# Optimization experiments

Hardware: AMD Instinct MI355X
Metric: run time of the kernel (lower is better)

Reference implementation:

```python
import jax, jax.numpy as jnp
import numpy as np


def setup_inputs() -> dict:
    key = jax.random.key(0)
    k0, k1, k2 = jax.random.split(key, 3)
    B, N, C = 2, 2048, 1024
    x = jax.random.normal(k0, (B, N, C), jnp.float32)
    W_qkv = jax.random.normal(k1, (3 * C, C), jnp.float32) * 0.02
    b_qkv = jnp.zeros((3 * C,), jnp.float32)
    W_out = jax.random.normal(k2, (C, C), jnp.float32) * 0.02
    b_out = jnp.zeros((C,), jnp.float32)
    return {"x": x, "W_qkv": W_qkv, "b_qkv": b_qkv, "W_out": W_out, "b_out": b_out, "n_heads": 16}


def reference(x, W_qkv, b_qkv, W_out, b_out, n_heads):
    B, N, C = x.shape
    dk = C // n_heads
    scale = 1.0 / np.sqrt(dk)
    # qkv projection -> (3, B, H, N, dk)
    qkv = (x @ W_qkv.T + b_qkv).reshape(B, N, 3, n_heads, dk).transpose(2, 0, 3, 1, 4)
    q, k, v = qkv[0], qkv[1], qkv[2]
    attn_all = jnp.einsum('bhqd,bhkd->bhqk', q, k) * scale  # (B,H,N,N)
    # sparsity measure per query row: max - mean
    M = jnp.max(attn_all, axis=-1) - jnp.mean(attn_all, axis=-1)  # (B,H,N)
    n_top = max(1, min(int(N * 0.25), N - 1))
    _, top_idx = jax.lax.top_k(M, n_top)  # (B,H,n_top)
    # keep[b,h,q] = True iff query row q is among top rows (vectorized scatter,
    # replaces the original per-(b,h) python loop)
    b_idx = jnp.arange(B)[:, None, None]
    h_idx = jnp.arange(n_heads)[None, :, None]
    keep = jnp.zeros((B, n_heads, N), bool).at[b_idx, h_idx, top_idx].set(True)
    # non-top query rows are fully masked to -1e9 (as in masked_fill)
    attn = jnp.where(keep[..., None], attn_all, jnp.float32(-1e9))
    attn = jax.nn.softmax(attn, axis=-1)
    # dropout is identity in eval mode
    out = jnp.einsum('bhqk,bhkd->bhqd', attn, v)
    out = out.transpose(0, 2, 1, 3).reshape(B, N, C)
    return out @ W_out.T + b_out
```

## Files before the change

kernel.cpp:

```cpp
#include <hip/hip_runtime.h>
#include <math.h>

typedef unsigned short u16;
typedef __attribute__((ext_vector_type(8))) short short8v;
typedef __attribute__((ext_vector_type(4))) float f32x4;

constexpr int B  = 2;
constexpr int N  = 2048;
constexpr int C  = 1024;
constexpr int H  = 16;
constexpr int DK = 64;
constexpr int NTOP = 512;
constexpr float SCALE = 0.125f;
constexpr int   BAND_CAP = 1024;
constexpr float BAND_EPS = 2e-3f;
constexpr int   CSEG = 16;

__device__ __forceinline__ void gload16(const u16* g, u16* l) {
    __builtin_amdgcn_global_load_lds(
        (const __attribute__((address_space(1))) unsigned int*)g,
        (__attribute__((address_space(3))) unsigned int*)l,
        16, 0, 0);
}

__device__ __forceinline__ u16 bf16_rne(float x) {
    unsigned u = __float_as_uint(x);
    unsigned r = u + 0x7fffu + ((u >> 16) & 1u);
    return (u16)(r >> 16);
}

__global__ __launch_bounds__(256) void convert_hilo(
    const float* __restrict__ src, u16* __restrict__ hi, u16* __restrict__ lo, int n)
{
    int i = (blockIdx.x * 256 + threadIdx.x) * 4;
    if (i >= n) return;
    float4 v = *(const float4*)&src[i];
    u16 h0 = bf16_rne(v.x), h1 = bf16_rne(v.y), h2 = bf16_rne(v.z), h3 = bf16_rne(v.w);
    float f0 = __uint_as_float((unsigned)h0 << 16);
    float f1 = __uint_as_float((unsigned)h1 << 16);
    float f2 = __uint_as_float((unsigned)h2 << 16);
    float f3 = __uint_as_float((unsigned)h3 << 16);
    *(ushort4*)&hi[i] = make_ushort4(h0, h1, h2, h3);
    *(ushort4*)&lo[i] = make_ushort4(bf16_rne(v.x - f0), bf16_rne(v.y - f1),
                                     bf16_rne(v.z - f2), bf16_rne(v.w - f3));
}

__global__ __launch_bounds__(256) void convert_hilo2(
    const float* __restrict__ a, const float* __restrict__ b,
    u16* __restrict__ ah, u16* __restrict__ al,
    u16* __restrict__ bh_, u16* __restrict__ bl_, int n)
{
    const float* src = blockIdx.y ? b : a;
    u16* hi = blockIdx.y ? bh_ : ah;
    u16* lo = blockIdx.y ? bl_ : al;
    int i = (blockIdx.x * 256 + threadIdx.x) * 4;
    if (i >= n) return;
    float4 v = *(const float4*)&src[i];
    u16 h0 = bf16_rne(v.x), h1 = bf16_rne(v.y), h2 = bf16_rne(v.z), h3 = bf16_rne(v.w);
    float f0 = __uint_as_float((unsigned)h0 << 16);
    float f1 = __uint_as_float((unsigned)h1 << 16);
    float f2 = __uint_as_float((unsigned)h2 << 16);
    float f3 = __uint_as_float((unsigned)h3 << 16);
    *(ushort4*)&hi[i] = make_ushort4(h0, h1, h2, h3);
    *(ushort4*)&lo[i] = make_ushort4(bf16_rne(v.x - f0), bf16_rne(v.y - f1),
                                     bf16_rne(v.z - f2), bf16_rne(v.w - f3));
}

__global__ __launch_bounds__(256) void convert_hilo_T(
    const float* __restrict__ v, u16* __restrict__ th, u16* __restrict__ tl)
{
    constexpr int LS = 68;
    __shared__ u16 Sh[64 * LS], Sl[64 * LS];
    const int bh = blockIdx.y;
    const int kt = blockIdx.x * 64;
    const int tid = threadIdx.x;
    #pragma unroll
    for (int p = 0; p < 4; ++p) {
        int idx = tid * 4 + p * 1024;
        int key = idx >> 6, d = idx & 63;
        float4 x4 = *(const float4*)&v[((size_t)bh * N + kt + key) * DK + d];
        float xs[4] = {x4.x, x4.y, x4.z, x4.w};
        ushort4 hh, ll;
        u16* hp = (u16*)&hh; u16* lp = (u16*)&ll;
        #pragma unroll
        for (int j = 0; j < 4; ++j) {
            u16 h = bf16_rne(xs[j]);
            hp[j] = h;
            lp[j] = bf16_rne(xs[j] - __uint_as_float((unsigned)h << 16));
        }
        *(ushort4*)&Sh[key * LS + d] = hh;
        *(ushort4*)&Sl[key * LS + d] = ll;
    }
    __syncthreads();
    const int d = tid >> 2, seg = tid & 3;
    u16 bufh[16], bufl[16];
    #pragma unroll
    for (int i = 0; i < 16; ++i) {
        bufh[i] = Sh[(seg * 16 + i) * LS + d];
        bufl[i] = Sl[(seg * 16 + i) * LS + d];
    }
    size_t oa = ((size_t)bh * DK + d) * N + kt + seg * 16;
    *(uint4*)&th[oa] = ((uint4*)bufh)[0];
    *(uint4*)&th[oa + 8] = ((uint4*)bufh)[1];
    *(uint4*)&tl[oa] = ((uint4*)bufl)[0];
    *(uint4*)&tl[oa + 8] = ((uint4*)bufl)[1];
}

template <int MODE>
__global__ __launch_bounds__(256) void gemm_mfma(
    const u16* __restrict__ Ahi, const u16* __restrict__ Alo,
    const u16* __restrict__ Bhi, const u16* __restrict__ Blo,
    const float* __restrict__ bias, float* __restrict__ out,
    float* __restrict__ qb, float* __restrict__ kb, float* __restrict__ vb,
    int K)
{
    __shared__ __align__(16) u16 Ah[128 * 32], Al[128 * 32];
    __shared__ __align__(16) u16 Bh[128 * 32], Bl[128 * 32];

    const int tid = threadIdx.x;
    const int m0 = blockIdx.y * 128;
    const int n0 = blockIdx.x * 128;
    const int lane = tid & 63;
    const int wave = tid >> 6;
    const int wr = wave >> 1, wc = wave & 1;
    const int fr = lane & 15, sl = lane >> 4;

    const u16* gsrc = (wave == 0) ? Ahi + (size_t)m0 * K
                    : (wave == 1) ? Alo + (size_t)m0 * K
                    : (wave == 2) ? Bhi + (size_t)n0 * K
                                  : Blo + (size_t)n0 * K;
    u16* lbase = (wave == 0) ? Ah : (wave == 1) ? Al : (wave == 2) ? Bh : Bl;

    f32x4 acc[4][4] = {};

    for (int k0 = 0; k0 < K; k0 += 32) {
        __syncthreads();
        #pragma unroll
        for (int i = 0; i < 8; ++i) {
            int c = i * 64 + lane;
            int row = c >> 2, sp = c & 3;
            int gs = sp ^ ((row >> 1) & 3);
            gload16(gsrc + (size_t)row * K + k0 + gs * 8, lbase + i * 512);
        }
        __syncthreads();

        short8v afh[4], afl[4], bfh[4], bfl[4];
        #pragma unroll
        for (int m = 0; m < 4; ++m) {
            int row = wr * 64 + m * 16 + fr;
            int off = row * 32 + ((sl ^ ((row >> 1) & 3)) * 8);
            afh[m] = *(const short8v*)&Ah[off];
            afl[m] = *(const short8v*)&Al[off];
        }
        #pragma unroll
        for (int n = 0; n < 4; ++n) {
            int row = wc * 64 + n * 16 + fr;
            int off = row * 32 + ((sl ^ ((row >> 1) & 3)) * 8);
            bfh[n] = *(const short8v*)&Bh[off];
            bfl[n] = *(const short8v*)&Bl[off];
        }
        #pragma unroll
        for (int m = 0; m < 4; ++m)
            #pragma unroll
            for (int n = 0; n < 4; ++n) {
                acc[m][n] = __builtin_amdgcn_mfma_f32_16x16x32_bf16(afh[m], bfh[n], acc[m][n], 0, 0, 0);
                acc[m][n] = __builtin_amdgcn_mfma_f32_16x16x32_bf16(afh[m], bfl[n], acc[m][n], 0, 0, 0);
                acc[m][n] = __builtin_amdgcn_mfma_f32_16x16x32_bf16(afl[m], bfh[n], acc[m][n], 0, 0, 0);
            }
    }

    #pragma unroll
    for (int m = 0; m < 4; ++m)
        #pragma unroll
        for (int n = 0; n < 4; ++n)
            #pragma unroll
            for (int r = 0; r < 4; ++r) {
                int grow = m0 + wr * 64 + m * 16 + sl * 4 + r;
                int gcol = n0 + wc * 64 + n * 16 + fr;
                float val = acc[m][n][r] + bias[gcol];
                if (MODE == 0) {
                    int t = gcol >> 10, h = (gcol >> 6) & 15, d = gcol & 63;
                    int bb = grow >> 11, nn = grow & (N - 1);
                    float* dst = (t == 0) ? qb : (t == 1) ? kb : vb;
                    dst[(((size_t)bb * H + h) * N + nn) * DK + d] = val;
                } else {
                    out[(size_t)grow * C + gcol] = val;
                }
            }
}

__global__ __launch_bounds__(256) void colsum_part2(
    const float* __restrict__ v, const float* __restrict__ k,
    float* __restrict__ partial)
{
    const int bh = blockIdx.y, seg = blockIdx.x, which = blockIdx.z;
    const float* src = which ? k : v;
    const int d = threadIdx.x & 63;
    const int sub = threadIdx.x >> 6;
    const int k0 = seg * (N / CSEG);
    float s = 0.f;
    for (int kk = sub; kk < N / CSEG; kk += 4)
        s += src[((size_t)bh * N + k0 + kk) * DK + d];
    __shared__ float part[4][64];
    part[sub][d] = s;
    __syncthreads();
    if (threadIdx.x < 64)
        partial[(((size_t)which * B * H + bh) * CSEG + seg) * DK + d] =
            part[0][d] + part[1][d] + part[2][d] + part[3][d];
}

__global__ __launch_bounds__(128) void colsum_final2(
    const float* __restrict__ partial, float* __restrict__ vmean,
    float* __restrict__ kmean)
{
    const int bh = blockIdx.x;
    const int d = threadIdx.x & 63;
    const int which = threadIdx.x >> 6;
    const float* p = partial + ((size_t)which * B * H + bh) * CSEG * DK;
    float s = 0.f;
    #pragma unroll
    for (int g = 0; g < CSEG; ++g) s += p[g * DK + d];
    float* dst = which ? kmean : vmean;
    dst[bh * DK + d] = s / (float)N;
}

__global__ __launch_bounds__(256) void qdot_kernel(
    const float* __restrict__ q, const float* __restrict__ kmean,
    float* __restrict__ Mdot)
{
    const int bh = blockIdx.y;
    const int row = blockIdx.x * 256 + threadIdx.x;
    __shared__ float km[DK];
    if (threadIdx.x < DK) km[threadIdx.x] = kmean[bh * DK + threadIdx.x];
    __syncthreads();
    const float* qr = &q[((size_t)bh * N + row) * DK];
    float s = 0.f;
    #pragma unroll
    for (int d4 = 0; d4 < DK; d4 += 4) {
        float4 v = *(const float4*)&qr[d4];
        s += v.x * km[d4] + v.y * km[d4 + 1] + v.z * km[d4 + 2] + v.w * km[d4 + 3];
    }
    Mdot[(size_t)bh * N + row] = s;
}

__global__ __launch_bounds__(256) void row_stats_mfma(
    const u16* __restrict__ qh_, const u16* __restrict__ ql_,
    const u16* __restrict__ kh_, const u16* __restrict__ kl_,
    const float* __restrict__ Mdot, float* __restrict__ Mout,
    float* __restrict__ rowmax)
{
    __shared__ __align__(16) u16 Kh[64 * 64];
    __shared__ __align__(16) u16 Kl[64 * 64];
    const int tid = threadIdx.x, lane = tid & 63, wave = tid >> 6;
    const int bh = blockIdx.y;
    const int q0 = blockIdx.x * 128 + wave * 32;
    const int fr = lane & 15, g = lane >> 4;

    const u16* gsrc = (wave & 2) ? kl_ : kh_;
    u16* lbase = (wave & 2) ? Kl : Kh;
    const int cb = (wave & 1) * 256;

    short8v qfh[2][2], qfl[2][2];
    #pragma unroll
    for (int m = 0; m < 2; ++m)
        #pragma unroll
        for (int kk = 0; kk < 2; ++kk) {
            size_t qa = ((size_t)bh * N + q0 + m * 16 + fr) * DK + kk * 32 + g * 8;
            qfh[m][kk] = *(const short8v*)&qh_[qa];
            qfl[m][kk] = *(const short8v*)&ql_[qa];
        }

    f32x4 mx[2];
    mx[0] = (f32x4){-1e30f, -1e30f, -1e30f, -1e30f};
    mx[1] = mx[0];

    for (int kt = 0; kt < N; kt += 64) {
        __syncthreads();
        #pragma unroll
        for (int i = 0; i < 4; ++i) {
            int c = cb + i * 64 + lane;
            int row = c >> 3, sp = c & 7;
            int gs = sp ^ (row & 7);
            gload16(gsrc + ((size_t)bh * N + kt + row) * DK + gs * 8,
                    lbase + (size_t)(cb + i * 64) * 8);
        }
        __syncthreads();
        short8v bfh[4][2], bfl[4][2];
        #pragma unroll
        for (int n = 0; n < 4; ++n)
            #pragma unroll
            for (int kk = 0; kk < 2; ++kk) {
                int key = n * 16 + fr;
                int off = key * 64 + (((g + kk * 4) ^ (key & 7)) * 8);
                bfh[n][kk] = *(const short8v*)&Kh[off];
                bfl[n][kk] = *(const short8v*)&Kl[off];
            }
        #pragma unroll
        for (int m = 0; m < 2; ++m)
            #pragma unroll
            for (int n = 0; n < 4; ++n) {
                f32x4 a = {};
                #pragma unroll
                for (int kk = 0; kk < 2; ++kk) {
                    a = __builtin_amdgcn_mfma_f32_16x16x32_bf16(qfl[m][kk], bfh[n][kk], a, 0, 0, 0);
                    a = __builtin_amdgcn_mfma_f32_16x16x32_bf16(qfh[m][kk], bfl[n][kk], a, 0, 0, 0);
                    a = __builtin_amdgcn_mfma_f32_16x16x32_bf16(qfh[m][kk], bfh[n][kk], a, 0, 0, 0);
                }
                #pragma unroll
                for (int r = 0; r < 4; ++r) mx[m][r] = fmaxf(mx[m][r], a[r]);
            }
    }

    #pragma unroll
    for (int w = 1; w < 16; w <<= 1)
        #pragma unroll
        for (int m = 0; m < 2; ++m)
            #pragma unroll
            for (int r = 0; r < 4; ++r)
                mx[m][r] = fmaxf(mx[m][r], __shfl_xor(mx[m][r], w, 64));

    if (fr == 0) {
        #pragma unroll
        for (int m = 0; m < 2; ++m)
            #pragma unroll
            for (int r = 0; r < 4; ++r) {
                int row = q0 + m * 16 + g * 4 + r;
                size_t idx = (size_t)bh * N + row;
                float v = mx[m][r];
                rowmax[idx] = SCALE * v;
                Mout[idx]   = SCALE * (v - Mdot[idx]);
            }
    }
}

__global__ __launch_bounds__(256) void topk_thr(
    const float* __restrict__ Mv, float* __restrict__ thr, int* __restrict__ cnt)
{
    const int bh = blockIdx.y;
    const int qi = blockIdx.x * 256 + threadIdx.x;
    if (blockIdx.x == 0 && threadIdx.x == 0) cnt[bh] = 0;
    __shared__ float Ms[N];
    for (int e = threadIdx.x; e < N; e += 256) Ms[e] = Mv[(size_t)bh * N + e];
    __syncthreads();
    const float mq = Ms[qi];
    int rank = 0;
    for (int j = 0; j < N; ++j) {
        float mj = Ms[j];
        rank += (mj > mq) || (mj == mq && j < qi);
    }
    if (rank == NTOP - 1) thr[bh] = mq;
}

__global__ __launch_bounds__(256) void band_classify(
    const float* __restrict__ Mv, const float* __restrict__ thr,
    int* __restrict__ cnt, int* __restrict__ band, int* __restrict__ keep)
{
    const int bh = blockIdx.y;
    const int row = blockIdx.x * 256 + threadIdx.x;
    const float m = Mv[(size_t)bh * N + row];
    const float t = thr[bh];
    int kp;
    if (fabsf(m - t) <= BAND_EPS) {
        int pos = atomicAdd(&cnt[bh], 1);
        if (pos < BAND_CAP) band[bh * BAND_CAP + pos] = row;
        kp = 0;
    } else {
        kp = (m > t) ? 1 : 0;
    }
    keep[(size_t)bh * N + row] = kp;
}

__global__ __launch_bounds__(256) void refine_kernel(
    const float* __restrict__ q, const float* __restrict__ k,
    const int* __restrict__ cnt, const int* __restrict__ band,
    float* __restrict__ Mv)
{
    constexpr int LS = 69;
    __shared__ float Ks[64 * LS];
    __shared__ float qs[DK];
    const int bh = blockIdx.y;
    const int tid = threadIdx.x;
    const int n = min(cnt[bh], BAND_CAP);
    for (int ci = blockIdx.x; ci < n; ci += 32) {
        const int row = band[bh * BAND_CAP + ci];
        __syncthreads();
        if (tid < DK) qs[tid] = q[((size_t)bh * N + row) * DK + tid];
        double mx = -1e30, sm = 0.0;
        for (int kt = 0; kt < N; kt += 64) {
            __syncthreads();
            #pragma unroll
            for (int p = 0; p < 4; ++p) {
                int idx = tid * 4 + p * 1024;
                int kr = idx >> 6, d = idx & 63;
                float4 x4 = *(const float4*)&k[((size_t)bh * N + kt + kr) * DK + d];
                Ks[kr * LS + d]     = x4.x;
                Ks[kr * LS + d + 1] = x4.y;
                Ks[kr * LS + d + 2] = x4.z;
                Ks[kr * LS + d + 3] = x4.w;
            }
            __syncthreads();
            if (tid < 64) {
                double s = 0.0;
                #pragma unroll
                for (int d = 0; d < DK; ++d)
                    s += (double)qs[d] * (double)Ks[tid * LS + d];
                mx = fmax(mx, s);
                sm += s;
            }
        }
        if (tid < 64) {
            #pragma unroll
            for (int w = 1; w < 64; w <<= 1) {
                mx = fmax(mx, __shfl_xor(mx, w, 64));
                sm += __shfl_xor(sm, w, 64);
            }
            if (tid == 0)
                Mv[(size_t)bh * N + row] = (float)((double)SCALE * (mx - sm / (double)N));
        }
    }
}

__global__ __launch_bounds__(256) void band_finalize(
    const float* __restrict__ Mv, const int* __restrict__ cnt,
    const int* __restrict__ band, int* __restrict__ keep,
    int* __restrict__ kidx)
{
    __shared__ unsigned char kL[N];
    __shared__ int   bRow[BAND_CAP];
    __shared__ float bM[BAND_CAP];
    __shared__ int aW[4];
    __shared__ int scan[256];

    const int bh = blockIdx.x;
    const int tid = threadIdx.x;
    const int lane = tid & 63, wid = tid >> 6;
    const int nb = min(cnt[bh], BAND_CAP);

    int above = 0;
    #pragma unroll
    for (int w = 0; w < 8; ++w) {
        int row = w * 256 + tid;
        int kp = keep[(size_t)bh * N + row];
        kL[row] = (unsigned char)kp;
        above += kp;
    }
    #pragma unroll
    for (int w = 1; w < 64; w <<= 1) above += __shfl_xor(above, w, 64);
    if (lane == 0) aW[wid] = above;
    for (int i = tid; i < nb; i += 256) {
        int r = band[bh * BAND_CAP + i];
        bRow[i] = r;
        bM[i] = Mv[(size_t)bh * N + r];
    }
    __syncthreads();
    const int nAbove = aW[0] + aW[1] + aW[2] + aW[3];

    for (int i = tid; i < nb; i += 256) {
        const float mi = bM[i];
        const int ri = bRow[i];
        int rank = nAbove;
        for (int j = 0; j < nb; ++j) {
            float mj = bM[j];
            rank += (mj > mi) || (mj == mi && bRow[j] < ri);
        }
        int kp = (rank < NTOP) ? 1 : 0;
        kL[ri] = (unsigned char)kp;
        keep[(size_t)bh * N + ri] = kp;
    }
    __syncthreads();

    int cntL = 0;
    #pragma unroll
    for (int r = 0; r < 8; ++r) cntL += kL[tid * 8 + r];
    scan[tid] = cntL;
    __syncthreads();
    for (int s = 1; s < 256; s <<= 1) {
        int v = (tid >= s) ? scan[tid - s] : 0;
        __syncthreads();
        scan[tid] += v;
        __syncthreads();
    }
    int pos = scan[tid] - cntL;
    #pragma unroll
    for (int r = 0; r < 8; ++r) {
        int row = tid * 8 + r;
        if (kL[row]) kidx[bh * NTOP + pos++] = row;
    }
}

__global__ __launch_bounds__(256) void fill_nonkept(
    const int* __restrict__ keep, const float* __restrict__ vmean,
    float* __restrict__ attn_out)
{
    const int bh = blockIdx.y;
    const int b = bh >> 4, h = bh & 15;
    const int d = threadIdx.x & 63;
    const int rr = threadIdx.x >> 6;
    const float vm = vmean[bh * DK + d];
    #pragma unroll
    for (int i = 0; i < 16; ++i) {
        int row = blockIdx.x * 64 + i * 4 + rr;
        if (!keep[(size_t)bh * N + row])
            attn_out[((size_t)b * N + row) * C + h * DK + d] = vm;
    }
}

__global__ __launch_bounds__(256) void attn_mfma(
    const u16* __restrict__ qh_, const u16* __restrict__ ql_,
    const u16* __restrict__ kh_, const u16* __restrict__ kl_,
    const u16* __restrict__ vth_, const u16* __restrict__ vtl_,
    const float* __restrict__ rowmax, const int* __restrict__ kidx,
    float* __restrict__ attn_out)
{
    __shared__ __align__(16) u16 Kh[64 * 64], Kl[64 * 64];
    __shared__ __align__(16) u16 Vh[64 * 64], Vl[64 * 64];
    __shared__ __align__(16) u16 Ph[4][16 * 64], Pl[4][16 * 64];

    const int tid = threadIdx.x, lane = tid & 63, wave = tid >> 6;
    const int wg = blockIdx.x;
    const int bh = ((wg >> 6) << 3) | (wg & 7);
    const int xblk = (wg >> 3) & 7;
    const int b = bh >> 4, h = bh & 15;
    const int q0 = xblk * 64 + wave * 16;
    const int fr = lane & 15, sl = lane >> 4;

    const bool isV = (wave >= 2);
    const u16* ksrc = (wave & 1) ? kl_ : kh_;
    const u16* vsrc = (wave & 1) ? vtl_ : vth_;
    u16* lbase = (wave == 0) ? Kh : (wave == 1) ? Kl : (wave == 2) ? Vh : Vl;
    const size_t kbase0 = (size_t)bh * N * DK;
    const size_t vbase0 = (size_t)bh * DK * N;

    const int* kix = kidx + bh * NTOP;
    const int qrow_f = kix[q0 + fr];
    int qr_o[4]; float rmax_r[4];
    #pragma unroll
    for (int r = 0; r < 4; ++r) {
        qr_o[r] = kix[q0 + sl * 4 + r];
        rmax_r[r] = rowmax[(size_t)bh * N + qr_o[r]];
    }

    short8v qfh[2], qfl[2];
    #pragma unroll
    for (int kk = 0; kk < 2; ++kk) {
        size_t qa = ((size_t)bh * N + qrow_f) * DK + kk * 32 + sl * 8;
        qfh[kk] = *(const short8v*)&qh_[qa];
        qfl[kk] = *(const short8v*)&ql_[qa];
    }

    f32x4 opv[4] = {};
    float lsum[4] = {};

    for (int kt = 0; kt < N; kt += 64) {
        __syncthreads();
        #pragma unroll
        for (int i = 0; i < 8; ++i) {
            int c = i * 64 + lane;
            int row = c >> 3, sp = c & 7;
            int gs = sp ^ (row & 7);
            const u16* g = isV ? (vsrc + vbase0 + (size_t)row * N + kt + gs * 8)
                               : (ksrc + kbase0 + (size_t)(kt + row) * DK + gs * 8);
            gload16(g, lbase + (size_t)i * 512);
        }
        __syncthreads();

        #pragma unroll
        for (int n = 0; n < 4; ++n) {
            f32x4 a = {};
            __builtin_amdgcn_s_setprio(1);
            #pragma unroll
            for (int kk = 0; kk < 2; ++kk) {
                int key = n * 16 + fr;
                int off = key * 64 + (((sl + kk * 4) ^ (key & 7)) * 8);
                short8v bh_f = *(const short8v*)&Kh[off];
                short8v bl_f = *(const short8v*)&Kl[off];
                a = __builtin_amdgcn_mfma_f32_16x16x32_bf16(qfl[kk], bh_f, a, 0, 0, 0);
                a = __builtin_amdgcn_mfma_f32_16x16x32_bf16(qfh[kk], bl_f, a, 0, 0, 0);
                a = __builtin_amdgcn_mfma_f32_16x16x32_bf16(qfh[kk], bh_f, a, 0, 0, 0);
            }
            __builtin_amdgcn_s_setprio(0);
            #pragma unroll
            for (int r = 0; r < 4; ++r) {
                float p = __expf(a[r] * SCALE - rmax_r[r]);
                lsum[r] += p;
                u16 ph = bf16_rne(p);
                u16 pl = bf16_rne(p - __uint_as_float((unsigned)ph << 16));
                int q_l = sl * 4 + r;
                int key = n * 16 + fr;
                int off = q_l * 64 + (((key >> 3) ^ (q_l & 7)) * 8) + (key & 7);
                Ph[wave][off] = ph;
                Pl[wave][off] = pl;
            }
        }

        __builtin_amdgcn_s_setprio(1);
        #pragma unroll
        for (int kk = 0; kk < 2; ++kk) {
            int aoff = fr * 64 + (((kk * 4 + sl) ^ (fr & 7)) * 8);
            short8v pah = *(const short8v*)&Ph[wave][aoff];
            short8v pal = *(const short8v*)&Pl[wave][aoff];
            #pragma unroll
            for (int n = 0; n < 4; ++n) {
                int d = n * 16 + fr;
                int voff = d * 64 + (((kk * 4 + sl) ^ (d & 7)) * 8);
                short8v vhf = *(const short8v*)&Vh[voff];
                short8v vlf = *(const short8v*)&Vl[voff];
                opv[n] = __builtin_amdgcn_mfma_f32_16x16x32_bf16(pal, vhf, opv[n], 0, 0, 0);
                opv[n] = __builtin_amdgcn_mfma_f32_16x16x32_bf16(pah, vlf, opv[n], 0, 0, 0);
                opv[n] = __builtin_amdgcn_mfma_f32_16x16x32_bf16(pah, vhf, opv[n], 0, 0, 0);
            }
        }
        __builtin_amdgcn_s_setprio(0);
    }

    #pragma unroll
    for (int w = 1; w < 16; w <<= 1)
        #pragma unroll
        for (int r = 0; r < 4; ++r)
            lsum[r] += __shfl_xor(lsum[r], w, 64);

    #pragma unroll
    for (int r = 0; r < 4; ++r) {
        const float inv = 1.0f / lsum[r];
        float* orow = attn_out + ((size_t)b * N + qr_o[r]) * C + h * DK;
        #pragma unroll
        for (int n = 0; n < 4; ++n)
            orow[n * 16 + fr] = opv[n][r] * inv;
    }
}

extern "C" void kernel_launch(void* const* d_in, const int* in_sizes, int n_in,
                              void* d_out, int out_size, void* d_ws, size_t ws_size,
                              hipStream_t stream)
{
    const float* x    = (const float*)d_in[0];
    const float* Wqkv = (const float*)d_in[1];
    const float* bqkv = (const float*)d_in[2];
    const float* Wout = (const float*)d_in[3];
    const float* bout = (const float*)d_in[4];
    float* out = (float*)d_out;

    char* ws = (char*)d_ws;
    size_t off = 0;
    auto alloc = [&](size_t bytes) -> void* {
        void* p = ws + off;
        off += (bytes + 255) & ~(size_t)255;
        return p;
    };

    const size_t BHND = (size_t)B * H * N * DK;
    float* q        = (float*)alloc(BHND * 4);
    float* kbuf     = (float*)alloc(BHND * 4);
    float* vbuf     = (float*)alloc(BHND * 4);
    float* attn_out = (float*)alloc((size_t)B * N * C * 4);
    u16* cvAhi = (u16*)alloc((size_t)B * N * C * 2);
    u16* cvAlo = (u16*)alloc((size_t)B * N * C * 2);
    u16* cvBhi = (u16*)alloc((size_t)3 * C * C * 2);
    u16* cvBlo = (u16*)alloc((size_t)3 * C * C * 2);
    u16* qhi   = (u16*)alloc(BHND * 2);
    u16* qlo   = (u16*)alloc(BHND * 2);
    u16* khi   = (u16*)alloc(BHND * 2);
    u16* klo   = (u16*)alloc(BHND * 2);
    u16* vthi  = (u16*)alloc(BHND * 2);
    u16* vtlo  = (u16*)alloc(BHND * 2);
    float* Mbuf     = (float*)alloc((size_t)B * H * N * 4);
    float* rmaxbuf  = (float*)alloc((size_t)B * H * N * 4);
    float* Mdot     = (float*)alloc((size_t)B * H * N * 4);
    int*   keep     = (int*)  alloc((size_t)B * H * N * 4);
    int*   kidx     = (int*)  alloc((size_t)B * H * NTOP * 4);
    float* vmeanbuf = (float*)alloc((size_t)B * H * DK * 4);
    float* kmeanbuf = (float*)alloc((size_t)B * H * DK * 4);
    float* partbuf  = (float*)alloc((size_t)2 * B * H * CSEG * DK * 4);
    float* thrbuf   = (float*)alloc((size_t)B * H * 4);
    int*   cntbuf   = (int*)  alloc((size_t)B * H * 4);
    int*   bandbuf  = (int*)  alloc((size_t)B * H * BAND_CAP * 4);

    const int nX = B * N * C;
    const int nW = 3 * C * C;
    const int nWo = C * C;

    convert_hilo<<<nX / 1024, 256, 0, stream>>>(x, cvAhi, cvAlo, nX);
    convert_hilo<<<nW / 1024, 256, 0, stream>>>(Wqkv, cvBhi, cvBlo, nW);

    gemm_mfma<0><<<dim3(3 * C / 128, (B * N) / 128), 256, 0, stream>>>(
        cvAhi, cvAlo, cvBhi, cvBlo, bqkv, nullptr, q, kbuf, vbuf, C);

    convert_hilo2<<<dim3(nX / 1024, 2), 256, 0, stream>>>(
        q, kbuf, qhi, qlo, khi, klo, nX);
    convert_hilo_T<<<dim3(N / 64, B * H), 256, 0, stream>>>(vbuf, vthi, vtlo);

    colsum_part2<<<dim3(CSEG, B * H, 2), 256, 0, stream>>>(vbuf, kbuf, partbuf);
    colsum_final2<<<B * H, 128, 0, stream>>>(partbuf, vmeanbuf, kmeanbuf);

    qdot_kernel<<<dim3(N / 256, B * H), 256, 0, stream>>>(q, kmeanbuf, Mdot);

    row_stats_mfma<<<dim3(N / 128, B * H), 256, 0, stream>>>(
        qhi, qlo, khi, klo, Mdot, Mbuf, rmaxbuf);

    topk_thr<<<dim3(N / 256, B * H), 256, 0, stream>>>(Mbuf, thrbuf, cntbuf);
    band_classify<<<dim3(N / 256, B * H), 256, 0, stream>>>(Mbuf, thrbuf, cntbuf, bandbuf, keep);
    refine_kernel<<<dim3(32, B * H), 256, 0, stream>>>(q, kbuf, cntbuf, bandbuf, Mbuf);
    band_finalize<<<B * H, 256, 0, stream>>>(Mbuf, cntbuf, bandbuf, keep, kidx);

    fill_nonkept<<<dim3(N / 64, B * H), 256, 0, stream>>>(keep, vmeanbuf, attn_out);
    attn_mfma<<<256, 256, 0, stream>>>(
        qhi, qlo, khi, klo, vthi, vtlo, rmaxbuf, kidx, attn_out);

    convert_hilo<<<nX / 1024, 256, 0, stream>>>(attn_out, cvAhi, cvAlo, nX);
    convert_hilo<<<nWo / 1024, 256, 0, stream>>>(Wout, cvBhi, cvBlo, nWo);
    gemm_mfma<1><<<dim3(C / 128, (B * N) / 128), 256, 0, stream>>>(
        cvAhi, cvAlo, cvBhi, cvBlo, bout, out, nullptr, nullptr, nullptr, C);
}
```

Before: 401.4 us.

## Split attention over key halves and merge partials in fused epilogue

The sparse attention kernel now splits the key range into two halves, launching 512 workgroups instead of 256, and writes unnormalised partial outputs and row sums. A new epilogue kernel combines the two halves, normalises them, and also fills the non-kept rows with the V mean, replacing the separate fill kernel. The split is meant to fill more compute units, since 256 workgroups underuse the device. In exchange it adds partial-buffer traffic, an inverse index map written by band_finalize, and one more kernel launch.

```diff
diff --git a/kernel.cpp b/kernel.cpp
--- a/kernel.cpp
+++ b/kernel.cpp
@@ -9,6 +9,7 @@
 constexpr int N  = 2048;
 constexpr int C  = 1024;
 constexpr int H  = 16;
+constexpr int BH = B * H;
 constexpr int DK = 64;
 constexpr int NTOP = 512;
 constexpr float SCALE = 0.125f;
@@ -205,7 +206,7 @@
     part[sub][d] = s;
     __syncthreads();
     if (threadIdx.x < 64)
-        partial[(((size_t)which * B * H + bh) * CSEG + seg) * DK + d] =
+        partial[(((size_t)which * BH + bh) * CSEG + seg) * DK + d] =
             part[0][d] + part[1][d] + part[2][d] + part[3][d];
 }
 
@@ -216,7 +217,7 @@
     const int bh = blockIdx.x;
     const int d = threadIdx.x & 63;
     const int which = threadIdx.x >> 6;
-    const float* p = partial + ((size_t)which * B * H + bh) * CSEG * DK;
+    const float* p = partial + ((size_t)which * BH + bh) * CSEG * DK;
     float s = 0.f;
     #pragma unroll
     for (int g = 0; g < CSEG; ++g) s += p[g * DK + d];
@@ -423,7 +424,7 @@
 __global__ __launch_bounds__(256) void band_finalize(
     const float* __restrict__ Mv, const int* __restrict__ cnt,
     const int* __restrict__ band, int* __restrict__ keep,
-    int* __restrict__ kidx)
+    int* __restrict__ kidx, int* __restrict__ inv)
 {
     __shared__ unsigned char kL[N];
     __shared__ int   bRow[BAND_CAP];
@@ -484,24 +485,11 @@
     #pragma unroll
     for (int r = 0; r < 8; ++r) {
         int row = tid * 8 + r;
-        if (kL[row]) kidx[bh * NTOP + pos++] = row;
-    }
-}
-
-__global__ __launch_bounds__(256) void fill_nonkept(
-    const int* __restrict__ keep, const float* __restrict__ vmean,
-    float* __restrict__ attn_out)
-{
-    const int bh = blockIdx.y;
-    const int b = bh >> 4, h = bh & 15;
-    const int d = threadIdx.x & 63;
-    const int rr = threadIdx.x >> 6;
-    const float vm = vmean[bh * DK + d];
-    #pragma unroll
-    for (int i = 0; i < 16; ++i) {
-        int row = blockIdx.x * 64 + i * 4 + rr;
-        if (!keep[(size_t)bh * N + row])
-            attn_out[((size_t)b * N + row) * C + h * DK + d] = vm;
+        if (kL[row]) {
+            kidx[bh * NTOP + pos] = row;
+            inv[(size_t)bh * N + row] = pos;
+            ++pos;
+        }
     }
 }
 
@@ -510,17 +498,18 @@
     const u16* __restrict__ kh_, const u16* __restrict__ kl_,
     const u16* __restrict__ vth_, const u16* __restrict__ vtl_,
     const float* __restrict__ rowmax, const int* __restrict__ kidx,
-    float* __restrict__ attn_out)
+    float* __restrict__ part_o, float* __restrict__ part_l)
 {
     __shared__ __align__(16) u16 Kh[64 * 64], Kl[64 * 64];
     __shared__ __align__(16) u16 Vh[64 * 64], Vl[64 * 64];
     __shared__ __align__(16) u16 Ph[4][16 * 64], Pl[4][16 * 64];
 
     const int tid = threadIdx.x, lane = tid & 63, wave = tid >> 6;
-    const int wg = blockIdx.x;
+    const int wg = blockIdx.x & 255;
+    const int half = blockIdx.x >> 8;
+    const int ks0 = half * (N / 2);
     const int bh = ((wg >> 6) << 3) | (wg & 7);
     const int xblk = (wg >> 3) & 7;
-    const int b = bh >> 4, h = bh & 15;
     const int q0 = xblk * 64 + wave * 16;
     const int fr = lane & 15, sl = lane >> 4;
 
@@ -533,12 +522,10 @@
 
     const int* kix = kidx + bh * NTOP;
     const int qrow_f = kix[q0 + fr];
-    int qr_o[4]; float rmax_r[4];
-    #pragma unroll
-    for (int r = 0; r < 4; ++r) {
-        qr_o[r] = kix[q0 + sl * 4 + r];
-        rmax_r[r] = rowmax[(size_t)bh * N + qr_o[r]];
-    }
+    float rmax_r[4];
+    #pragma unroll
+    for (int r = 0; r < 4; ++r)
+        rmax_r[r] = rowmax[(size_t)bh * N + kix[q0 + sl * 4 + r]];
 
     short8v qfh[2], qfl[2];
     #pragma unroll
@@ -551,7 +538,7 @@
     f32x4 opv[4] = {};
     float lsum[4] = {};
 
-    for (int kt = 0; kt < N; kt += 64) {
+    for (int kt = ks0; kt < ks0 + N / 2; kt += 64) {
         __syncthreads();
         #pragma unroll
         for (int i = 0; i < 8; ++i) {
@@ -619,13 +606,40 @@
         for (int r = 0; r < 4; ++r)
             lsum[r] += __shfl_xor(lsum[r], w, 64);
 
+    const size_t pbase = ((size_t)half * BH + bh) * NTOP;
     #pragma unroll
     for (int r = 0; r < 4; ++r) {
-        const float inv = 1.0f / lsum[r];
-        float* orow = attn_out + ((size_t)b * N + qr_o[r]) * C + h * DK;
+        const int pos = q0 + sl * 4 + r;
+        if (fr == 0) part_l[pbase + pos] = lsum[r];
         #pragma unroll
         for (int n = 0; n < 4; ++n)
-            orow[n * 16 + fr] = opv[n][r] * inv;
+            part_o[(pbase + pos) * DK + n * 16 + fr] = opv[n][r];
+    }
+}
+
+__global__ __launch_bounds__(256) void attn_epilogue(
+    const float* __restrict__ part_o, const float* __restrict__ part_l,
+    const int* __restrict__ keep, const int* __restrict__ inv,
+    const float* __restrict__ vmean, float* __restrict__ attn_out)
+{
+    const int bh = blockIdx.y;
+    const int b = bh >> 4, h = bh & 15;
+    const int r0 = blockIdx.x * 128;
+    const int tid = threadIdx.x;
+    for (int e = tid; e < 128 * DK; e += 256) {
+        const int row = r0 + (e >> 6);
+        const int d = e & 63;
+        float o;
+        if (keep[(size_t)bh * N + row]) {
+            const int pos = inv[(size_t)bh * N + row];
+            const size_t p0 = ((size_t)0 * BH + bh) * NTOP + pos;
+            const size_t p1 = ((size_t)1 * BH + bh) * NTOP + pos;
+            const float l = part_l[p0] + part_l[p1];
+            o = (part_o[p0 * DK + d] + part_o[p1 * DK + d]) / l;
+        } else {
+            o = vmean[bh * DK + d];
+        }
+        attn_out[((size_t)b * N + row) * C + h * DK + d] = o;
     }
 }
 
@@ -663,17 +677,20 @@
     u16* klo   = (u16*)alloc(BHND * 2);
     u16* vthi  = (u16*)alloc(BHND * 2);
     u16* vtlo  = (u16*)alloc(BHND * 2);
-    float* Mbuf     = (float*)alloc((size_t)B * H * N * 4);
-    float* rmaxbuf  = (float*)alloc((size_t)B * H * N * 4);
-    float* Mdot     = (float*)alloc((size_t)B * H * N * 4);
-    int*   keep     = (int*)  alloc((size_t)B * H * N * 4);
-    int*   kidx     = (int*)  alloc((size_t)B * H * NTOP * 4);
-    float* vmeanbuf = (float*)alloc((size_t)B * H * DK * 4);
-    float* kmeanbuf = (float*)alloc((size_t)B * H * DK * 4);
-    float* partbuf  = (float*)alloc((size_t)2 * B * H * CSEG * DK * 4);
-    float* thrbuf   = (float*)alloc((size_t)B * H * 4);
-    int*   cntbuf   = (int*)  alloc((size_t)B * H * 4);
-    int*   bandbuf  = (int*)  alloc((size_t)B * H * BAND_CAP * 4);
+    float* Mbuf     = (float*)alloc((size_t)BH * N * 4);
+    float* rmaxbuf  = (float*)alloc((size_t)BH * N * 4);
+    float* Mdot     = (float*)alloc((size_t)BH * N * 4);
+    int*   keep     = (int*)  alloc((size_t)BH * N * 4);
+    int*   inv      = (int*)  alloc((size_t)BH * N * 4);
+    int*   kidx     = (int*)  alloc((size_t)BH * NTOP * 4);
+    float* vmeanbuf = (float*)alloc((size_t)BH * DK * 4);
+    float* kmeanbuf = (float*)alloc((size_t)BH * DK * 4);
+    float* partbuf  = (float*)alloc((size_t)2 * BH * CSEG * DK * 4);
+    float* thrbuf   = (float*)alloc((size_t)BH * 4);
+    int*   cntbuf   = (int*)  alloc((size_t)BH * 4);
+    int*   bandbuf  = (int*)  alloc((size_t)BH * BAND_CAP * 4);
+    float* part_o   = (float*)alloc((size_t)2 * BH * NTOP * DK * 4);
+    float* part_l   = (float*)alloc((size_t)2 * BH * NTOP * 4);
 
     const int nX = B * N * C;
     const int nW = 3 * C * C;
@@ -687,24 +704,25 @@
 
     convert_hilo2<<<dim3(nX / 1024, 2), 256, 0, stream>>>(
         q, kbuf, qhi, qlo, khi, klo, nX);
-    convert_hilo_T<<<dim3(N / 64, B * H), 256, 0, stream>>>(vbuf, vthi, vtlo);
-
-    colsum_part2<<<dim3(CSEG, B * H, 2), 256, 0, stream>>>(vbuf, kbuf, partbuf);
-    colsum_final2<<<B * H, 128, 0, stream>>>(partbuf, vmeanbuf, kmeanbuf);
-
-    qdot_kernel<<<dim3(N / 256, B * H), 256, 0, stream>>>(q, kmeanbuf, Mdot);
-
-    row_stats_mfma<<<dim3(N / 128, B * H), 256, 0, stream>>>(
+    convert_hilo_T<<<dim3(N / 64, BH), 256, 0, stream>>>(vbuf, vthi, vtlo);
+
+    colsum_part2<<<dim3(CSEG, BH, 2), 256, 0, stream>>>(vbuf, kbuf, partbuf);
+    colsum_final2<<<BH, 128, 0, stream>>>(partbuf, vmeanbuf, kmeanbuf);
+
+    qdot_kernel<<<dim3(N / 256, BH), 256, 0, stream>>>(q, kmeanbuf, Mdot);
+
+    row_stats_mfma<<<dim3(N / 128, BH), 256, 0, stream>>>(
         qhi, qlo, khi, klo, Mdot, Mbuf, rmaxbuf);
 
-    topk_thr<<<dim3(N / 256, B * H), 256, 0, stream>>>(Mbuf, thrbuf, cntbuf);
-    band_classify<<<dim3(N / 256, B * H), 256, 0, stream>>>(Mbuf, thrbuf, cntbuf, bandbuf, keep);
-    refine_kernel<<<dim3(32, B * H), 256, 0, stream>>>(q, kbuf, cntbuf, bandbuf, Mbuf);
-    band_finalize<<<B * H, 256, 0, stream>>>(Mbuf, cntbuf, bandbuf, keep, kidx);
-
-    fill_nonkept<<<dim3(N / 64, B * H), 256, 0, stream>>>(keep, vmeanbuf, attn_out);
-    attn_mfma<<<256, 256, 0, stream>>>(
-        qhi, qlo, khi, klo, vthi, vtlo, rmaxbuf, kidx, attn_out);
+    topk_thr<<<dim3(N / 256, BH), 256, 0, stream>>>(Mbuf, thrbuf, cntbuf);
+    band_classify<<<dim3(N / 256, BH), 256, 0, stream>>>(Mbuf, thrbuf, cntbuf, bandbuf, keep);
+    refine_kernel<<<dim3(32, BH), 256, 0, stream>>>(q, kbuf, cntbuf, bandbuf, Mbuf);
+    band_finalize<<<BH, 256, 0, stream>>>(Mbuf, cntbuf, bandbuf, keep, kidx, inv);
+
+    attn_mfma<<<512, 256, 0, stream>>>(
+        qhi, qlo, khi, klo, vthi, vtlo, rmaxbuf, kidx, part_o, part_l);
+    attn_epilogue<<<dim3(16, BH), 256, 0, stream>>>(
+        part_o, part_l, keep, inv, vmeanbuf, attn_out);
 
     convert_hilo<<<nX / 1024, 256, 0, stream>>>(attn_out, cvAhi, cvAlo, nX);
     convert_hilo<<<nWo / 1024, 256, 0, stream>>>(Wout, cvBhi, cvBlo, nWo);
```

Result: no change. 395.4 us (-1.5%).
